# Performance work log

Hardware: AMD Instinct MI355X
Metric: run time of the kernel (lower is better)

## Reference

```python
import jax, jax.numpy as jnp
import numpy as np

TEMPERATURE = 0.02
B, T, D = 32, 256, 128


def _l2norm(x):
    return x / jnp.linalg.norm(x, axis=-1, keepdims=True)


def setup_inputs() -> dict:
    key = jax.random.key(0)
    k1, k2, k3, k4, k5, k6 = jax.random.split(key, 6)
    query_single = _l2norm(jax.random.normal(k1, (B, D), dtype=jnp.float32))
    pos_single = _l2norm(jax.random.normal(k2, (B, D), dtype=jnp.float32))
    query_multi = _l2norm(jax.random.normal(k3, (B, T, D), dtype=jnp.float32))
    pos_multi = _l2norm(jax.random.normal(k4, (B, T, D), dtype=jnp.float32))
    # variable-length masks (at least 1 valid token each, like real tokenized batches)
    q_len = jax.random.randint(k5, (B,), T // 4, T + 1)
    p_len = jax.random.randint(k6, (B,), T // 4, T + 1)
    pos = jnp.arange(T)[None, :]
    q_mask = pos < q_len[:, None]
    p_mask = pos < p_len[:, None]
    return {
        "query_single": query_single,
        "pos_single": pos_single,
        "query_multi": query_multi,
        "pos_multi": pos_multi,
        "q_mask": q_mask,
        "p_mask": p_mask,
    }


def _late_interaction_similarity(q_tokens, q_mask, p_tokens, p_mask):
    # All-pairs token similarity: [Bq, Bp, Tq, Tp]
    sim = jnp.einsum("bqd,cpd->bcqp", q_tokens, p_tokens)
    neg = jnp.finfo(sim.dtype).min
    sim = jnp.where(p_mask[None, :, None, :], sim, neg)
    mx = jnp.max(sim, axis=-1)                       # [Bq, Bp, Tq]
    mx = jnp.where(q_mask[:, None, :], mx, 0.0)      # drop invalid query tokens
    s = jnp.sum(mx, axis=-1)                         # [Bq, Bp]
    t_i = jnp.maximum(jnp.sum(q_mask, axis=-1), 1).astype(sim.dtype)  # [Bq]
    return s / t_i[:, None]


def _diag_cross_entropy(logits):
    # labels = arange(B): standard in-batch InfoNCE
    logp = jax.nn.log_softmax(logits, axis=-1)
    return -jnp.mean(jnp.diagonal(logp))


def reference(query_single, pos_single, query_multi, pos_multi, q_mask, p_mask):
    tau = TEMPERATURE
    dense_sim = query_single @ pos_single.T                       # [B, B]
    single_loss = _diag_cross_entropy(dense_sim / tau)

    S_late = _late_interaction_similarity(query_multi, q_mask, pos_multi, p_mask)
    multi_loss = _diag_cross_entropy(S_late / tau)

    dense_probs = jax.nn.softmax(dense_sim / tau, axis=1)
    late_probs = jax.nn.softmax(S_late / tau, axis=1)
    eps = 1e-8
    kl = jnp.mean(jnp.sum(dense_probs * jnp.log((dense_probs + eps) / (late_probs + eps)), axis=1))

    total_loss = single_loss + multi_loss + kl
    return (total_loss, single_loss, multi_loss, kl)
```

## Files before the change

### kernel.cpp

```cpp
#include <hip/hip_runtime.h>
#include <hip/hip_bf16.h>

#define B_SZ 32
#define T_SZ 256
#define D_SZ 128
#define TAU_INV 50.0f

typedef __bf16 bf16x8 __attribute__((ext_vector_type(8)));
typedef float f32x4 __attribute__((ext_vector_type(4)));

__device__ __forceinline__ unsigned short f2bf(float f) {
    union { float f; unsigned int u; } v; v.f = f;
    unsigned int r = v.u + 0x7fffu + ((v.u >> 16) & 1u);
    return (unsigned short)(r >> 16);
}

__device__ __forceinline__ bool mask_is_byte(const void* m) {
    return ((const int*)m)[0] != 1;
}
__device__ __forceinline__ int mget(const void* m, int idx, bool isb) {
    return isb ? (((const unsigned char*)m)[idx] != 0) : (((const int*)m)[idx] != 0);
}

__global__ __launch_bounds__(256) void cvt_both(
    const float* __restrict__ qsrc, const float* __restrict__ psrc,
    unsigned short* __restrict__ Qb, unsigned short* __restrict__ Pb) {
    const int half = blockIdx.x >> 10;
    const float* s = half ? psrc : qsrc;
    unsigned short* d = half ? Pb : Qb;
    int i = ((blockIdx.x & 1023) * 256 + threadIdx.x) * 4;
    float4 v = *(const float4*)(s + i);
    ushort4 o;
    o.x = f2bf(v.x); o.y = f2bf(v.y); o.z = f2bf(v.z); o.w = f2bf(v.w);
    *(ushort4*)(d + i) = o;
}

__global__ __launch_bounds__(512, 4) void late_sim(
    const unsigned short* __restrict__ Qbf, const unsigned short* __restrict__ Pbf,
    const void* __restrict__ qmask, const void* __restrict__ pmask,
    float* __restrict__ sraw)
{
    __shared__ __align__(16) unsigned char Plds[T_SZ * D_SZ * 2];
    __shared__ float madd[T_SZ];
    __shared__ float qmul[2][T_SZ];
    __shared__ float wsum[2][8];

    const int tid = threadIdx.x;
    const int l   = tid & 63;
    const int w   = tid >> 6;
    const int bid = blockIdx.x;
    const int c   = bid & 31;
    const int bg  = bid >> 5;
    const int b0  = bg, b1 = bg + 16;
    const int lr  = l & 15;
    const int lg  = l >> 4;

    const bool isb = mask_is_byte(qmask);
    const unsigned short* Pc = Pbf + c * (T_SZ * D_SZ);

    #pragma unroll
    for (int it = 0; it < 8; ++it) {
        int m   = it * 512 + tid;
        int row = m >> 4;
        int cs  = m & 15;
        bf16x8 v = *(const bf16x8*)(Pc + m * 8);
        *(bf16x8*)(Plds + row * 256 + ((cs ^ (row & 7)) << 4)) = v;
    }
    {
        int t = tid & 255;
        if (tid < 256) madd[t] = mget(pmask, c * T_SZ + t, isb) ? 0.0f : -1e30f;
        qmul[tid >> 8][t] = mget(qmask, (tid < 256 ? b0 : b1) * T_SZ + t, isb) ? 1.0f : 0.0f;
    }

    bf16x8 qf0[2][4], qf1[2][4];
    #pragma unroll
    for (int qt = 0; qt < 2; ++qt)
        #pragma unroll
        for (int k = 0; k < 4; ++k) {
            int roff = (w * 32 + qt * 16 + lr) * D_SZ + k * 32 + lg * 8;
            qf0[qt][k] = *(const bf16x8*)(Qbf + b0 * (T_SZ * D_SZ) + roff);
            qf1[qt][k] = *(const bf16x8*)(Qbf + b1 * (T_SZ * D_SZ) + roff);
        }

    __syncthreads();

    float r00 = -3e38f, r01 = -3e38f, r10 = -3e38f, r11 = -3e38f;

    for (int pt = 0; pt < 16; ++pt) {
        f32x4 a00 = {0,0,0,0}, a01 = {0,0,0,0}, a10 = {0,0,0,0}, a11 = {0,0,0,0};
        #pragma unroll
        for (int k = 0; k < 4; ++k) {
            int row = pt * 16 + lr;
            bf16x8 af = *(const bf16x8*)(Plds + row * 256 + (((k * 4 + lg) ^ (row & 7)) << 4));
            a00 = __builtin_amdgcn_mfma_f32_16x16x32_bf16(af, qf0[0][k], a00, 0, 0, 0);
            a01 = __builtin_amdgcn_mfma_f32_16x16x32_bf16(af, qf0[1][k], a01, 0, 0, 0);
            a10 = __builtin_amdgcn_mfma_f32_16x16x32_bf16(af, qf1[0][k], a10, 0, 0, 0);
            a11 = __builtin_amdgcn_mfma_f32_16x16x32_bf16(af, qf1[1][k], a11, 0, 0, 0);
        }
        float pm0 = madd[pt * 16 + lg * 4 + 0];
        float pm1 = madd[pt * 16 + lg * 4 + 1];
        float pm2 = madd[pt * 16 + lg * 4 + 2];
        float pm3 = madd[pt * 16 + lg * 4 + 3];
        r00 = fmaxf(r00, fmaxf(fmaxf(a00[0]+pm0, a00[1]+pm1), fmaxf(a00[2]+pm2, a00[3]+pm3)));
        r01 = fmaxf(r01, fmaxf(fmaxf(a01[0]+pm0, a01[1]+pm1), fmaxf(a01[2]+pm2, a01[3]+pm3)));
        r10 = fmaxf(r10, fmaxf(fmaxf(a10[0]+pm0, a10[1]+pm1), fmaxf(a10[2]+pm2, a10[3]+pm3)));
        r11 = fmaxf(r11, fmaxf(fmaxf(a11[0]+pm0, a11[1]+pm1), fmaxf(a11[2]+pm2, a11[3]+pm3)));
    }

    r00 = fmaxf(r00, __shfl_xor(r00, 16)); r00 = fmaxf(r00, __shfl_xor(r00, 32));
    r01 = fmaxf(r01, __shfl_xor(r01, 16)); r01 = fmaxf(r01, __shfl_xor(r01, 32));
    r10 = fmaxf(r10, __shfl_xor(r10, 16)); r10 = fmaxf(r10, __shfl_xor(r10, 32));
    r11 = fmaxf(r11, __shfl_xor(r11, 16)); r11 = fmaxf(r11, __shfl_xor(r11, 32));

    float t0 = r00 * qmul[0][w * 32 + lr] + r01 * qmul[0][w * 32 + 16 + lr];
    float t1 = r10 * qmul[1][w * 32 + lr] + r11 * qmul[1][w * 32 + 16 + lr];
    #pragma unroll
    for (int off = 32; off > 0; off >>= 1) {
        t0 += __shfl_down(t0, off);
        t1 += __shfl_down(t1, off);
    }
    if (l == 0) { wsum[0][w] = t0 * 0.25f; wsum[1][w] = t1 * 0.25f; }
    __syncthreads();

    if (tid == 0) {
        float s0 = 0.f, s1 = 0.f;
        #pragma unroll
        for (int ww = 0; ww < 8; ++ww) { s0 += wsum[0][ww]; s1 += wsum[1][ww]; }
        sraw[b0 * 32 + c] = s0;
        sraw[b1 * 32 + c] = s1;
    }
}

__global__ __launch_bounds__(256) void loss_final(
    const float* __restrict__ qs, const float* __restrict__ ps,
    const float* __restrict__ sraw, const void* __restrict__ qmask,
    float* __restrict__ out)
{
    __shared__ float qsL[B_SZ * 132];
    __shared__ float psL[B_SZ * 132];
    __shared__ float dense[B_SZ * B_SZ];
    __shared__ float late[B_SZ * B_SZ];
    __shared__ float tcnt[B_SZ];
    __shared__ float rsA[B_SZ], rmA[B_SZ], rkA[B_SZ];

    const int tid = threadIdx.x;
    const bool isb = mask_is_byte(qmask);

    for (int i = tid; i < 1024; i += 256) {
        int r = i >> 5, c4 = (i & 31) * 4;
        *(float4*)(qsL + r * 132 + c4) = *(const float4*)(qs + r * D_SZ + c4);
        *(float4*)(psL + r * 132 + c4) = *(const float4*)(ps + r * D_SZ + c4);
    }
    {
        const int r = tid >> 3, j = tid & 7;
        int cnt = 0;
        if (isb) {
            const unsigned int* mm = (const unsigned int*)((const unsigned char*)qmask + r * T_SZ + j * 32);
            #pragma unroll
            for (int t = 0; t < 8; ++t) cnt += (int)((mm[t] * 0x01010101u) >> 24);
        } else {
            const int* mm = (const int*)qmask + r * T_SZ + j * 32;
            #pragma unroll
            for (int t = 0; t < 32; ++t) cnt += (mm[t] != 0);
        }
        cnt += __shfl_xor(cnt, 1);
        cnt += __shfl_xor(cnt, 2);
        cnt += __shfl_xor(cnt, 4);
        if (j == 0) tcnt[r] = (float)(cnt > 1 ? cnt : 1);
    }
    __syncthreads();

    for (int idx = tid; idx < B_SZ * B_SZ; idx += 256) {
        int r = idx >> 5, cc = idx & 31;
        float s = 0.f;
        #pragma unroll
        for (int i = 0; i < D_SZ; i += 4) {
            float4 a  = *(const float4*)(qsL + r  * 132 + i);
            float4 bb = *(const float4*)(psL + cc * 132 + i);
            s += a.x * bb.x + a.y * bb.y + a.z * bb.z + a.w * bb.w;
        }
        dense[r * 32 + cc] = s;
        late[r * 32 + cc]  = sraw[idx] / tcnt[r];
    }
    __syncthreads();

    {
        const int cc = tid & 31;
        #pragma unroll
        for (int it = 0; it < 4; ++it) {
            const int r = (tid >> 5) + 8 * it;
            float xd = dense[r * 32 + cc] * TAU_INV;
            float xl = late[r * 32 + cc]  * TAU_INV;
            float md = xd, ml = xl;
            #pragma unroll
            for (int off = 16; off > 0; off >>= 1) {
                md = fmaxf(md, __shfl_xor(md, off));
                ml = fmaxf(ml, __shfl_xor(ml, off));
            }
            float sd = expf(xd - md), sl = expf(xl - ml);
            #pragma unroll
            for (int off = 16; off > 0; off >>= 1) {
                sd += __shfl_xor(sd, off);
                sl += __shfl_xor(sl, off);
            }
            float lsd = md + logf(sd);
            float lsl = ml + logf(sl);
            float pd = expf(xd - lsd);
            float pl = expf(xl - lsl);
            float klt = pd * logf((pd + 1e-8f) / (pl + 1e-8f));
            #pragma unroll
            for (int off = 16; off > 0; off >>= 1) klt += __shfl_xor(klt, off);
            if (cc == 0) rkA[r] = klt;
            if (cc == r) { rsA[r] = -(xd - lsd); rmA[r] = -(xl - lsl); }
        }
    }
    __syncthreads();

    if (tid < B_SZ) {
        float a = rsA[tid], bb = rmA[tid], c2 = rkA[tid];
        #pragma unroll
        for (int off = 16; off > 0; off >>= 1) {
            a  += __shfl_xor(a, off);
            bb += __shfl_xor(bb, off);
            c2 += __shfl_xor(c2, off);
        }
        if (tid == 0) {
            a *= (1.0f / B_SZ); bb *= (1.0f / B_SZ); c2 *= (1.0f / B_SZ);
            out[0] = a + bb + c2;
            out[1] = a;
            out[2] = bb;
            out[3] = c2;
        }
    }
}

extern "C" void kernel_launch(void* const* d_in, const int* in_sizes, int n_in,
                              void* d_out, int out_size, void* d_ws, size_t ws_size,
                              hipStream_t stream) {
    const float* qs    = (const float*)d_in[0];
    const float* ps    = (const float*)d_in[1];
    const float* qm3   = (const float*)d_in[2];
    const float* pm3   = (const float*)d_in[3];
    const void*  qmask = d_in[4];
    const void*  pmask = d_in[5];
    float* out = (float*)d_out;

    const int NTOK = B_SZ * T_SZ * D_SZ;
    unsigned short* Qbf = (unsigned short*)d_ws;
    unsigned short* Pbf = Qbf + NTOK;
    float* sraw = (float*)(Pbf + NTOK);

    cvt_both<<<2048, 256, 0, stream>>>(qm3, pm3, Qbf, Pbf);
    late_sim<<<512, 512, 0, stream>>>(Qbf, Pbf, qmask, pmask, sraw);
    loss_final<<<1, 256, 0, stream>>>(qs, ps, sraw, qmask, out);
}
```

Before: 39.52 us.

## Double-buffer P tile in LDS with chunked prefetch overlapping MFMA compute

Replaces the single up-front 64 KB LDS staging of the passage tokens with a two-buffer, 64-row-chunk pipeline. The next chunk's global loads are issued before computing on the current chunk and stored to the other buffer afterwards. This aims to hide global load latency behind MFMA work and halve LDS use, which could allow more resident blocks. Only one barrier per chunk is used, placed after the write, so a fast wave may overwrite a buffer another wave is still reading (a write-after-read race risk).

```diff
diff --git a/kernel.cpp b/kernel.cpp
--- a/kernel.cpp
+++ b/kernel.cpp
@@ -40,7 +40,7 @@
     const void* __restrict__ qmask, const void* __restrict__ pmask,
     float* __restrict__ sraw)
 {
-    __shared__ __align__(16) unsigned char Plds[T_SZ * D_SZ * 2];
+    __shared__ __align__(16) unsigned char Plds[2][64 * 256];
     __shared__ float madd[T_SZ];
     __shared__ float qmul[2][T_SZ];
     __shared__ float wsum[2][8];
@@ -58,14 +58,15 @@
     const bool isb = mask_is_byte(qmask);
     const unsigned short* Pc = Pbf + c * (T_SZ * D_SZ);
 
-    #pragma unroll
-    for (int it = 0; it < 8; ++it) {
-        int m   = it * 512 + tid;
-        int row = m >> 4;
-        int cs  = m & 15;
-        bf16x8 v = *(const bf16x8*)(Pc + m * 8);
-        *(bf16x8*)(Plds + row * 256 + ((cs ^ (row & 7)) << 4)) = v;
-    }
+    const int m0 = tid, m1 = 512 + tid;
+    const int r0 = m0 >> 4, cs0 = m0 & 15;
+    const int r1 = m1 >> 4, cs1 = m1 & 15;
+    const int w0 = r0 * 256 + ((cs0 ^ (r0 & 7)) << 4);
+    const int w1 = r1 * 256 + ((cs1 ^ (r1 & 7)) << 4);
+
+    const bf16x8* src0 = (const bf16x8*)Pc;
+    bf16x8 p0 = src0[m0], p1 = src0[m1];
+
     {
         int t = tid & 255;
         if (tid < 256) madd[t] = mget(pmask, c * T_SZ + t, isb) ? 0.0f : -1e30f;
@@ -82,29 +83,48 @@
             qf1[qt][k] = *(const bf16x8*)(Qbf + b1 * (T_SZ * D_SZ) + roff);
         }
 
+    *(bf16x8*)(Plds[0] + w0) = p0;
+    *(bf16x8*)(Plds[0] + w1) = p1;
     __syncthreads();
 
     float r00 = -3e38f, r01 = -3e38f, r10 = -3e38f, r11 = -3e38f;
 
-    for (int pt = 0; pt < 16; ++pt) {
-        f32x4 a00 = {0,0,0,0}, a01 = {0,0,0,0}, a10 = {0,0,0,0}, a11 = {0,0,0,0};
-        #pragma unroll
-        for (int k = 0; k < 4; ++k) {
-            int row = pt * 16 + lr;
-            bf16x8 af = *(const bf16x8*)(Plds + row * 256 + (((k * 4 + lg) ^ (row & 7)) << 4));
-            a00 = __builtin_amdgcn_mfma_f32_16x16x32_bf16(af, qf0[0][k], a00, 0, 0, 0);
-            a01 = __builtin_amdgcn_mfma_f32_16x16x32_bf16(af, qf0[1][k], a01, 0, 0, 0);
-            a10 = __builtin_amdgcn_mfma_f32_16x16x32_bf16(af, qf1[0][k], a10, 0, 0, 0);
-            a11 = __builtin_amdgcn_mfma_f32_16x16x32_bf16(af, qf1[1][k], a11, 0, 0, 0);
-        }
-        float pm0 = madd[pt * 16 + lg * 4 + 0];
-        float pm1 = madd[pt * 16 + lg * 4 + 1];
-        float pm2 = madd[pt * 16 + lg * 4 + 2];
-        float pm3 = madd[pt * 16 + lg * 4 + 3];
-        r00 = fmaxf(r00, fmaxf(fmaxf(a00[0]+pm0, a00[1]+pm1), fmaxf(a00[2]+pm2, a00[3]+pm3)));
-        r01 = fmaxf(r01, fmaxf(fmaxf(a01[0]+pm0, a01[1]+pm1), fmaxf(a01[2]+pm2, a01[3]+pm3)));
-        r10 = fmaxf(r10, fmaxf(fmaxf(a10[0]+pm0, a10[1]+pm1), fmaxf(a10[2]+pm2, a10[3]+pm3)));
-        r11 = fmaxf(r11, fmaxf(fmaxf(a11[0]+pm0, a11[1]+pm1), fmaxf(a11[2]+pm2, a11[3]+pm3)));
+    #pragma unroll
+    for (int ch = 0; ch < 4; ++ch) {
+        bf16x8 s0, s1;
+        if (ch < 3) {
+            const bf16x8* src = (const bf16x8*)(Pc + (ch + 1) * (64 * D_SZ));
+            s0 = src[m0]; s1 = src[m1];
+        }
+        const unsigned char* buf = Plds[ch & 1];
+        #pragma unroll
+        for (int ptl = 0; ptl < 4; ++ptl) {
+            f32x4 a00 = {0,0,0,0}, a01 = {0,0,0,0}, a10 = {0,0,0,0}, a11 = {0,0,0,0};
+            #pragma unroll
+            for (int k = 0; k < 4; ++k) {
+                int lrow = ptl * 16 + lr;
+                bf16x8 af = *(const bf16x8*)(buf + lrow * 256 + (((k * 4 + lg) ^ (lrow & 7)) << 4));
+                a00 = __builtin_amdgcn_mfma_f32_16x16x32_bf16(af, qf0[0][k], a00, 0, 0, 0);
+                a01 = __builtin_amdgcn_mfma_f32_16x16x32_bf16(af, qf0[1][k], a01, 0, 0, 0);
+                a10 = __builtin_amdgcn_mfma_f32_16x16x32_bf16(af, qf1[0][k], a10, 0, 0, 0);
+                a11 = __builtin_amdgcn_mfma_f32_16x16x32_bf16(af, qf1[1][k], a11, 0, 0, 0);
+            }
+            int grow = ch * 64 + ptl * 16 + lg * 4;
+            float pm0 = madd[grow + 0];
+            float pm1 = madd[grow + 1];
+            float pm2 = madd[grow + 2];
+            float pm3 = madd[grow + 3];
+            r00 = fmaxf(r00, fmaxf(fmaxf(a00[0]+pm0, a00[1]+pm1), fmaxf(a00[2]+pm2, a00[3]+pm3)));
+            r01 = fmaxf(r01, fmaxf(fmaxf(a01[0]+pm0, a01[1]+pm1), fmaxf(a01[2]+pm2, a01[3]+pm3)));
+            r10 = fmaxf(r10, fmaxf(fmaxf(a10[0]+pm0, a10[1]+pm1), fmaxf(a10[2]+pm2, a10[3]+pm3)));
+            r11 = fmaxf(r11, fmaxf(fmaxf(a11[0]+pm0, a11[1]+pm1), fmaxf(a11[2]+pm2, a11[3]+pm3)));
+        }
+        if (ch < 3) {
+            unsigned char* nbuf = Plds[(ch + 1) & 1];
+            *(bf16x8*)(nbuf + w0) = s0;
+            *(bf16x8*)(nbuf + w1) = s1;
+            __syncthreads();
+        }
     }
 
     r00 = fmaxf(r00, __shfl_xor(r00, 16)); r00 = fmaxf(r00, __shfl_xor(r00, 32));
```

Measured after the change: 39.40 us. About the same (-0.3%).
